# Kernel tuning notes

Measured on AMD Instinct MI355X. Metric: run time of the kernel, lower is better.

Reference implementation:

```python
import jax, jax.numpy as jnp
import numpy as np

NUM_ITERATIONS = 3


def squash(s, axis):
    # s: capsule vectors; squash along `axis` (capsule dim)
    mag_sq = jnp.sum(s * s, axis=axis, keepdims=True)
    mag = jnp.sqrt(mag_sq)
    return mag_sq / (1.0 + mag_sq) * (s / mag)


def setup_inputs() -> dict:
    key = jax.random.key(0)
    k1, k2 = jax.random.split(key)
    B, IN_SIZE, I = 256, 8, 1152   # batch, in_size, in_node_num
    N, O = 10, 16                  # num_node, node_size
    x = jax.random.normal(k1, (B, IN_SIZE, I), dtype=jnp.float32)
    W = jax.random.normal(k2, (1, I, N, O, IN_SIZE), dtype=jnp.float32)
    return {"x": x, "W": W}


def reference(x, W):
    # x: (B, in_size, I); W: (1, I, N, O, in_size)
    B = x.shape[0]
    I, N = W.shape[1], W.shape[2]
    xt = jnp.swapaxes(x, 1, 2)  # (B, I, in_size)
    # u_hat[b,i,n,o] = sum_k (0.03*W[0,i,n,o,k]) * x[b,i,k]
    u_hat = jnp.einsum('inok,bik->bino', W[0] * 0.03, xt)  # (B, I, N, O)
    b_ij = jnp.zeros((I, N), dtype=x.dtype)
    v_j = None
    for _ in range(NUM_ITERATIONS):
        c_ij = jax.nn.softmax(b_ij, axis=1)              # softmax over num_node
        s_j = jnp.einsum('in,bino->bno', c_ij, u_hat)    # (B, N, O)
        v_j = squash(s_j, axis=-1)                       # squash over node_size
        # agreement: u_hat . v_j, averaged over batch
        u_vj = jnp.einsum('bino,bno->bin', u_hat, v_j).mean(axis=0)  # (I, N)
        b_ij = b_ij + u_vj
    return v_j[:, :, :, None]  # (B, N, O, 1) == v_j.squeeze(1) in torch
```

## Files before the change

### kernel.cpp

```cpp
#include <hip/hip_runtime.h>

#define B_   256
#define I_   1152
#define N_   10
#define P_   9216
#define NO_  160

typedef unsigned short u16;
typedef short s8v __attribute__((ext_vector_type(8)));
typedef float f4v __attribute__((ext_vector_type(4)));

__device__ inline float bf2f(u16 u){
  unsigned v = ((unsigned)u) << 16; float f; __builtin_memcpy(&f, &v, 4); return f;
}
__device__ inline u16 f2bf(float f){
  unsigned b; __builtin_memcpy(&b, &f, 4);
  b += 0x7fffu + ((b >> 16) & 1u);
  return (u16)(b >> 16);
}

__global__ void k_prep(const float* __restrict__ x, const float* __restrict__ W,
                       u16* __restrict__ xbp, u16* __restrict__ xpb,
                       u16* __restrict__ Wt, float* __restrict__ bij){
  __shared__ float tile[32][36];
  int t = threadIdx.x, u = blockIdx.x;
  if (u < 160){
    if (u < 45) bij[u*256 + t] = 0.f;
    int q = u, n = q >> 4, o = q & 15;
    for (int i0 = 0; i0 < I_; i0 += 256){
      int i = i0 + t;
      if (i < I_){
        const float* src = W + (size_t)i*1280 + n*128 + o*8;
        float4 a = *reinterpret_cast<const float4*>(src);
        float4 b = *reinterpret_cast<const float4*>(src + 4);
        float vv[8] = {a.x,a.y,a.z,a.w,b.x,b.y,b.z,b.w};
        #pragma unroll
        for (int k = 0; k < 8; ++k)
          Wt[(size_t)q*P_ + (size_t)k*I_ + i] = f2bf(vv[k] * 0.03f);
      }
    }
  } else {
    int b2 = u - 160;
    int tb = b2 & 7, tp = b2 >> 3;
    int b0 = tb << 5, p0 = tp << 5;
    int r = t >> 3, c4 = (t & 7) << 2;
    float4 v = *reinterpret_cast<const float4*>(x + (size_t)(b0 + r)*P_ + p0 + c4);
    *reinterpret_cast<float4*>(&tile[r][c4]) = v;
    uint2 pk;
    pk.x = (unsigned)f2bf(v.x) | ((unsigned)f2bf(v.y) << 16);
    pk.y = (unsigned)f2bf(v.z) | ((unsigned)f2bf(v.w) << 16);
    *reinterpret_cast<uint2*>(xbp + (size_t)(b0 + r)*P_ + p0 + c4) = pk;
    __syncthreads();
    float f0 = tile[c4+0][r], f1 = tile[c4+1][r], f2 = tile[c4+2][r], f3 = tile[c4+3][r];
    uint2 pk2;
    pk2.x = (unsigned)f2bf(f0) | ((unsigned)f2bf(f1) << 16);
    pk2.y = (unsigned)f2bf(f2) | ((unsigned)f2bf(f3) << 16);
    *reinterpret_cast<uint2*>(xpb + (size_t)(p0 + r)*B_ + b0 + c4) = pk2;
  }
}

__global__ __launch_bounds__(128) void k_s2(
    const u16* __restrict__ xbp, const u16* __restrict__ Wt,
    const float* __restrict__ bij, float* __restrict__ s_part){
  __shared__ u16  Bt[16][584];
  __shared__ float c_lds[576];
  int t = threadIdx.x;
  int bx2 = blockIdx.x, n = blockIdx.y, kc = blockIdx.z;
  int i0 = (kc & 1) * 576;

  for (int j = t; j < 576; j += 128){
    const float* br = bij + (size_t)(i0 + j)*N_;
    float l0 = br[0], l1 = br[1], l2 = br[2], l3 = br[3], l4 = br[4];
    float l5 = br[5], l6 = br[6], l7 = br[7], l8 = br[8], l9 = br[9];
    float mx = fmaxf(fmaxf(fmaxf(fmaxf(l0,l1),fmaxf(l2,l3)),
                           fmaxf(fmaxf(l4,l5),fmaxf(l6,l7))), fmaxf(l8,l9));
    float e0=__expf(l0-mx), e1=__expf(l1-mx), e2=__expf(l2-mx), e3=__expf(l3-mx), e4=__expf(l4-mx);
    float e5=__expf(l5-mx), e6=__expf(l6-mx), e7=__expf(l7-mx), e8=__expf(l8-mx), e9=__expf(l9-mx);
    float se = e0+e1+e2+e3+e4+e5+e6+e7+e8+e9;
    float ev[10] = {e0,e1,e2,e3,e4,e5,e6,e7,e8,e9};
    c_lds[j] = ev[n] / se;
  }
  __syncthreads();

  for (int u = t; u < 1152; u += 128){
    int r = u / 72, cb = (u - r*72) * 8;
    uint4 w = *reinterpret_cast<const uint4*>(Wt + (size_t)(n*16 + r)*P_ + kc*576 + cb);
    float4 c0 = *reinterpret_cast<const float4*>(&c_lds[cb]);
    float4 c1 = *reinterpret_cast<const float4*>(&c_lds[cb + 4]);
    uint4 rr;
    rr.x = (unsigned)f2bf(bf2f(w.x & 0xffff)*c0.x) | ((unsigned)f2bf(bf2f(w.x >> 16)*c0.y) << 16);
    rr.y = (unsigned)f2bf(bf2f(w.y & 0xffff)*c0.z) | ((unsigned)f2bf(bf2f(w.y >> 16)*c0.w) << 16);
    rr.z = (unsigned)f2bf(bf2f(w.z & 0xffff)*c1.x) | ((unsigned)f2bf(bf2f(w.z >> 16)*c1.y) << 16);
    rr.w = (unsigned)f2bf(bf2f(w.w & 0xffff)*c1.z) | ((unsigned)f2bf(bf2f(w.w >> 16)*c1.w) << 16);
    *reinterpret_cast<uint4*>(&Bt[r][cb]) = rr;
  }
  __syncthreads();

  int w = t >> 6, l = t & 63;
  int lo = l & 15, quad = l >> 4;
  int b0 = bx2*32 + w*16;
  const s8v* ap = reinterpret_cast<const s8v*>(xbp + (size_t)(b0 + lo)*P_ + kc*576 + quad*8);
  f4v acc0 = {0.f,0.f,0.f,0.f}, acc1 = {0.f,0.f,0.f,0.f};
  #pragma unroll
  for (int s = 0; s < 9; ++s){
    s8v a0 = ap[8*s];
    s8v b0v = *reinterpret_cast<const s8v*>(&Bt[lo][quad*8 + 64*s]);
    s8v a1 = ap[8*s + 4];
    s8v b1v = *reinterpret_cast<const s8v*>(&Bt[lo][quad*8 + 64*s + 32]);
    acc0 = __builtin_amdgcn_mfma_f32_16x16x32_bf16(a0, b0v, acc0, 0, 0, 0);
    acc1 = __builtin_amdgcn_mfma_f32_16x16x32_bf16(a1, b1v, acc1, 0, 0, 0);
  }
  f4v acc = acc0 + acc1;
  float* op = s_part + (size_t)kc*40960;
  int r0 = quad << 2;
  #pragma unroll
  for (int r = 0; r < 4; ++r)
    op[(size_t)(b0 + r0 + r)*NO_ + n*16 + lo] = acc[r];
}

__global__ void k_sq(const float* __restrict__ s_part, float* __restrict__ out,
                     u16* __restrict__ vbt){
  int t = threadIdx.x;
  int o = t & 15, rl = t >> 4;
  int rowid = blockIdx.x*16 + rl;
  int b = rowid / 10, n = rowid - b*10;
  size_t idx = (size_t)b*NO_ + n*16 + o;
  float sv = 0.f;
  #pragma unroll
  for (int c = 0; c < 16; ++c) sv += s_part[idx + (size_t)c*40960];
  float sq = sv * sv;
  #pragma unroll
  for (int m = 8; m >= 1; m >>= 1) sq += __shfl_xor(sq, m, 16);
  float outv = sv * sqrtf(sq) / (1.0f + sq);
  out[idx] = outv;
  vbt[(size_t)(n*16 + o)*B_ + b] = f2bf(outv);
}

__global__ void k_g(const u16* __restrict__ xpb, const u16* __restrict__ vbt,
                    const u16* __restrict__ Wt, float* __restrict__ bij){
  int w = blockIdx.x*4 + (threadIdx.x >> 6);
  int l = threadIdx.x & 63;
  int pt = w % 576, qp = w / 576;
  int p0 = pt << 4;
  int lo = l & 15, quad = l >> 4;
  const s8v* ap  = reinterpret_cast<const s8v*>(xpb + (size_t)(p0 + lo)*B_ + quad*8);
  const s8v* bp0 = reinterpret_cast<const s8v*>(vbt + (size_t)((qp*2+0)*16 + lo)*B_ + quad*8);
  const s8v* bp1 = reinterpret_cast<const s8v*>(vbt + (size_t)((qp*2+1)*16 + lo)*B_ + quad*8);
  f4v acc0 = {0.f,0.f,0.f,0.f}, acc1 = {0.f,0.f,0.f,0.f};
  #pragma unroll
  for (int s = 0; s < 8; ++s){
    s8v a  = ap[4*s];
    s8v b0 = bp0[4*s];
    s8v b1 = bp1[4*s];
    acc0 = __builtin_amdgcn_mfma_f32_16x16x32_bf16(a, b0, acc0, 0, 0, 0);
    acc1 = __builtin_amdgcn_mfma_f32_16x16x32_bf16(a, b1, acc1, 0, 0, 0);
  }
  int ib = p0 % 1152;
  #pragma unroll
  for (int s = 0; s < 2; ++s){
    f4v acc = s ? acc1 : acc0;
    int n = qp*2 + s;
    const u16* wp = Wt + (size_t)(n*16 + lo)*P_ + p0 + (quad << 2);
    ushort4 w4 = *reinterpret_cast<const ushort4*>(wp);
    float v0 = acc[0]*bf2f(w4.x), v1 = acc[1]*bf2f(w4.y);
    float v2 = acc[2]*bf2f(w4.z), v3 = acc[3]*bf2f(w4.w);
    #pragma unroll
    for (int m = 8; m >= 1; m >>= 1){
      v0 += __shfl_xor(v0, m, 16);
      v1 += __shfl_xor(v1, m, 16);
      v2 += __shfl_xor(v2, m, 16);
      v3 += __shfl_xor(v3, m, 16);
    }
    if (lo == 0){
      int i = ib + (quad << 2);
      atomicAdd(&bij[(i+0)*N_ + n], v0 * (1.f/256.f));
      atomicAdd(&bij[(i+1)*N_ + n], v1 * (1.f/256.f));
      atomicAdd(&bij[(i+2)*N_ + n], v2 * (1.f/256.f));
      atomicAdd(&bij[(i+3)*N_ + n], v3 * (1.f/256.f));
    }
  }
}

extern "C" void kernel_launch(void* const* d_in, const int* in_sizes, int n_in,
                              void* d_out, int out_size, void* d_ws, size_t ws_size,
                              hipStream_t stream){
  (void)in_sizes; (void)n_in; (void)out_size; (void)ws_size;
  const float* x = (const float*)d_in[0];
  const float* W = (const float*)d_in[1];
  float* out = (float*)d_out;

  float* s_part = (float*)d_ws;
  float* bij    = s_part + 16*40960;
  u16* xbp = (u16*)(bij + 11520);
  u16* xpb = xbp + 2359296;
  u16* Wt  = xpb + 2359296;
  u16* vbt = Wt  + 1474560;

  k_prep<<<2464, 256, 0, stream>>>(x, W, xbp, xpb, Wt, bij);
  for (int it = 0; it < 3; ++it){
    k_s2<<<dim3(8, 10, 16), 128, 0, stream>>>(xbp, Wt, bij, s_part);
    k_sq<<<160, 256, 0, stream>>>(s_part, out, vbt);
    if (it < 2)
      k_g<<<720, 256, 0, stream>>>(xpb, vbt, Wt, bij);
  }
}
```

Measured before the change: 143.2 us.

## Process two capsule nodes per s2 block and split W prep across more blocks

k_s2 now computes two output nodes per block, so each A fragment loaded from global xbp is reused for two sets of MFMAs. This halves the number of blocks and the redundant softmax and x traffic. k_prep splits each W row's transpose over five blocks instead of one looping block, which should give more parallelism in the prep phase. In exchange, LDS per block roughly doubles and the grid shrinks to 640 blocks, which may reduce occupancy and latency hiding.

```diff
diff --git a/kernel.cpp b/kernel.cpp
--- a/kernel.cpp
+++ b/kernel.cpp
@@ -24,23 +24,22 @@
                        u16* __restrict__ Wt, float* __restrict__ bij){
   __shared__ float tile[32][36];
   int t = threadIdx.x, u = blockIdx.x;
-  if (u < 160){
+  if (u < 800){
     if (u < 45) bij[u*256 + t] = 0.f;
-    int q = u, n = q >> 4, o = q & 15;
-    for (int i0 = 0; i0 < I_; i0 += 256){
-      int i = i0 + t;
-      if (i < I_){
-        const float* src = W + (size_t)i*1280 + n*128 + o*8;
-        float4 a = *reinterpret_cast<const float4*>(src);
-        float4 b = *reinterpret_cast<const float4*>(src + 4);
-        float vv[8] = {a.x,a.y,a.z,a.w,b.x,b.y,b.z,b.w};
-        #pragma unroll
-        for (int k = 0; k < 8; ++k)
-          Wt[(size_t)q*P_ + (size_t)k*I_ + i] = f2bf(vv[k] * 0.03f);
-      }
+    int q = u / 5, ic = u - (u/5)*5;
+    int n = q >> 4, o = q & 15;
+    int i = ic*256 + t;
+    if (i < I_){
+      const float* src = W + (size_t)i*1280 + n*128 + o*8;
+      float4 a = *reinterpret_cast<const float4*>(src);
+      float4 b = *reinterpret_cast<const float4*>(src + 4);
+      float vv[8] = {a.x,a.y,a.z,a.w,b.x,b.y,b.z,b.w};
+      #pragma unroll
+      for (int k = 0; k < 8; ++k)
+        Wt[(size_t)q*P_ + (size_t)k*I_ + i] = f2bf(vv[k] * 0.03f);
     }
   } else {
-    int b2 = u - 160;
+    int b2 = u - 800;
     int tb = b2 & 7, tp = b2 >> 3;
     int b0 = tb << 5, p0 = tp << 5;
     int r = t >> 3, c4 = (t & 7) << 2;
@@ -62,10 +61,10 @@
 __global__ __launch_bounds__(128) void k_s2(
     const u16* __restrict__ xbp, const u16* __restrict__ Wt,
     const float* __restrict__ bij, float* __restrict__ s_part){
-  __shared__ u16  Bt[16][584];
-  __shared__ float c_lds[576];
+  __shared__ u16  Bt[2][16][592];
+  __shared__ float c2[2][576];
   int t = threadIdx.x;
-  int bx2 = blockIdx.x, n = blockIdx.y, kc = blockIdx.z;
+  int bx2 = blockIdx.x, np = blockIdx.y, kc = blockIdx.z;
   int i0 = (kc & 1) * 576;
 
   for (int j = t; j < 576; j += 128){
@@ -77,22 +76,26 @@
     float e0=__expf(l0-mx), e1=__expf(l1-mx), e2=__expf(l2-mx), e3=__expf(l3-mx), e4=__expf(l4-mx);
     float e5=__expf(l5-mx), e6=__expf(l6-mx), e7=__expf(l7-mx), e8=__expf(l8-mx), e9=__expf(l9-mx);
     float se = e0+e1+e2+e3+e4+e5+e6+e7+e8+e9;
+    float inv = 1.f / se;
     float ev[10] = {e0,e1,e2,e3,e4,e5,e6,e7,e8,e9};
-    c_lds[j] = ev[n] / se;
+    c2[0][j] = ev[np*2]   * inv;
+    c2[1][j] = ev[np*2+1] * inv;
   }
   __syncthreads();
 
-  for (int u = t; u < 1152; u += 128){
-    int r = u / 72, cb = (u - r*72) * 8;
-    uint4 w = *reinterpret_cast<const uint4*>(Wt + (size_t)(n*16 + r)*P_ + kc*576 + cb);
-    float4 c0 = *reinterpret_cast<const float4*>(&c_lds[cb]);
-    float4 c1 = *reinterpret_cast<const float4*>(&c_lds[cb + 4]);
+  for (int u = t; u < 2304; u += 128){
+    int nn = u / 1152, rem = u - nn*1152;
+    int r = rem / 72, cb = (rem - r*72) * 8;
+    int q = (np*2 + nn)*16 + r;
+    uint4 w = *reinterpret_cast<const uint4*>(Wt + (size_t)q*P_ + kc*576 + cb);
+    float4 c0 = *reinterpret_cast<const float4*>(&c2[nn][cb]);
+    float4 c1 = *reinterpret_cast<const float4*>(&c2[nn][cb + 4]);
     uint4 rr;
     rr.x = (unsigned)f2bf(bf2f(w.x & 0xffff)*c0.x) | ((unsigned)f2bf(bf2f(w.x >> 16)*c0.y) << 16);
     rr.y = (unsigned)f2bf(bf2f(w.y & 0xffff)*c0.z) | ((unsigned)f2bf(bf2f(w.y >> 16)*c0.w) << 16);
     rr.z = (unsigned)f2bf(bf2f(w.z & 0xffff)*c1.x) | ((unsigned)f2bf(bf2f(w.z >> 16)*c1.y) << 16);
     rr.w = (unsigned)f2bf(bf2f(w.w & 0xffff)*c1.z) | ((unsigned)f2bf(bf2f(w.w >> 16)*c1.w) << 16);
-    *reinterpret_cast<uint4*>(&Bt[r][cb]) = rr;
+    *reinterpret_cast<uint4*>(&Bt[nn][r][cb]) = rr;
   }
   __syncthreads();
 
@@ -100,22 +103,30 @@
   int lo = l & 15, quad = l >> 4;
   int b0 = bx2*32 + w*16;
   const s8v* ap = reinterpret_cast<const s8v*>(xbp + (size_t)(b0 + lo)*P_ + kc*576 + quad*8);
-  f4v acc0 = {0.f,0.f,0.f,0.f}, acc1 = {0.f,0.f,0.f,0.f};
+  f4v a00 = {0.f,0.f,0.f,0.f}, a01 = {0.f,0.f,0.f,0.f};
+  f4v a10 = {0.f,0.f,0.f,0.f}, a11 = {0.f,0.f,0.f,0.f};
   #pragma unroll
   for (int s = 0; s < 9; ++s){
-    s8v a0 = ap[8*s];
-    s8v b0v = *reinterpret_cast<const s8v*>(&Bt[lo][quad*8 + 64*s]);
-    s8v a1 = ap[8*s + 4];
-    s8v b1v = *reinterpret_cast<const s8v*>(&Bt[lo][quad*8 + 64*s + 32]);
-    acc0 = __builtin_amdgcn_mfma_f32_16x16x32_bf16(a0, b0v, acc0, 0, 0, 0);
-    acc1 = __builtin_amdgcn_mfma_f32_16x16x32_bf16(a1, b1v, acc1, 0, 0, 0);
-  }
-  f4v acc = acc0 + acc1;
+    s8v av0 = ap[8*s];
+    s8v av1 = ap[8*s + 4];
+    s8v b00 = *reinterpret_cast<const s8v*>(&Bt[0][lo][quad*8 + 64*s]);
+    s8v b01 = *reinterpret_cast<const s8v*>(&Bt[0][lo][quad*8 + 64*s + 32]);
+    s8v b10 = *reinterpret_cast<const s8v*>(&Bt[1][lo][quad*8 + 64*s]);
+    s8v b11 = *reinterpret_cast<const s8v*>(&Bt[1][lo][quad*8 + 64*s + 32]);
+    a00 = __builtin_amdgcn_mfma_f32_16x16x32_bf16(av0, b00, a00, 0, 0, 0);
+    a01 = __builtin_amdgcn_mfma_f32_16x16x32_bf16(av1, b01, a01, 0, 0, 0);
+    a10 = __builtin_amdgcn_mfma_f32_16x16x32_bf16(av0, b10, a10, 0, 0, 0);
+    a11 = __builtin_amdgcn_mfma_f32_16x16x32_bf16(av1, b11, a11, 0, 0, 0);
+  }
+  f4v accA = a00 + a01;
+  f4v accB = a10 + a11;
   float* op = s_part + (size_t)kc*40960;
   int r0 = quad << 2;
   #pragma unroll
-  for (int r = 0; r < 4; ++r)
-    op[(size_t)(b0 + r0 + r)*NO_ + n*16 + lo] = acc[r];
+  for (int r = 0; r < 4; ++r){
+    op[(size_t)(b0 + r0 + r)*NO_ + (np*2+0)*16 + lo] = accA[r];
+    op[(size_t)(b0 + r0 + r)*NO_ + (np*2+1)*16 + lo] = accB[r];
+  }
 }
 
 __global__ void k_sq(const float* __restrict__ s_part, float* __restrict__ out,
@@ -196,9 +207,9 @@
   u16* Wt  = xpb + 2359296;
   u16* vbt = Wt  + 1474560;
 
-  k_prep<<<2464, 256, 0, stream>>>(x, W, xbp, xpb, Wt, bij);
+  k_prep<<<3104, 256, 0, stream>>>(x, W, xbp, xpb, Wt, bij);
   for (int it = 0; it < 3; ++it){
-    k_s2<<<dim3(8, 10, 16), 128, 0, stream>>>(xbp, Wt, bij, s_part);
+    k_s2<<<dim3(8, 5, 16), 128, 0, stream>>>(xbp, Wt, bij, s_part);
     k_sq<<<160, 256, 0, stream>>>(s_part, out, vbt);
     if (it < 2)
       k_g<<<720, 256, 0, stream>>>(xpb, vbt, Wt, bij);
```

Result: slower. 148.6 us (+3.8%).

## Fuse squash into agreement kernel and reduce s partials with atomics

Applied to the files above, without the earlier changes.

The s_j partial sums are now accumulated with atomicAdd into a single double-buffered s array instead of 16 partial slices. Each s2 launch zeroes the next buffer, and the standalone squash kernel is removed from the loop. The agreement kernel computes the squash itself and stages v in LDS as bf16. The W prep is spread over more blocks. This cuts kernel launches and the extra partial-sum traffic, at the cost of atomic contention and redundant squash work repeated in every k_g2 block.

```diff
diff --git a/kernel.cpp b/kernel.cpp
--- a/kernel.cpp
+++ b/kernel.cpp
@@ -21,26 +21,27 @@
 
 __global__ void k_prep(const float* __restrict__ x, const float* __restrict__ W,
                        u16* __restrict__ xbp, u16* __restrict__ xpb,
-                       u16* __restrict__ Wt, float* __restrict__ bij){
+                       u16* __restrict__ Wt, float* __restrict__ bij,
+                       float* __restrict__ sA){
   __shared__ float tile[32][36];
   int t = threadIdx.x, u = blockIdx.x;
-  if (u < 160){
+  if (u < 800){
     if (u < 45) bij[u*256 + t] = 0.f;
-    int q = u, n = q >> 4, o = q & 15;
-    for (int i0 = 0; i0 < I_; i0 += 256){
-      int i = i0 + t;
-      if (i < I_){
-        const float* src = W + (size_t)i*1280 + n*128 + o*8;
-        float4 a = *reinterpret_cast<const float4*>(src);
-        float4 b = *reinterpret_cast<const float4*>(src + 4);
-        float vv[8] = {a.x,a.y,a.z,a.w,b.x,b.y,b.z,b.w};
-        #pragma unroll
-        for (int k = 0; k < 8; ++k)
-          Wt[(size_t)q*P_ + (size_t)k*I_ + i] = f2bf(vv[k] * 0.03f);
-      }
+    else if (u < 205) sA[(u - 45)*256 + t] = 0.f;
+    int q = u / 5, ic = u - (u/5)*5;
+    int n = q >> 4, o = q & 15;
+    int i = ic*256 + t;
+    if (i < I_){
+      const float* src = W + (size_t)i*1280 + n*128 + o*8;
+      float4 a = *reinterpret_cast<const float4*>(src);
+      float4 b = *reinterpret_cast<const float4*>(src + 4);
+      float vv[8] = {a.x,a.y,a.z,a.w,b.x,b.y,b.z,b.w};
+      #pragma unroll
+      for (int k = 0; k < 8; ++k)
+        Wt[(size_t)q*P_ + (size_t)k*I_ + i] = f2bf(vv[k] * 0.03f);
     }
   } else {
-    int b2 = u - 160;
+    int b2 = u - 800;
     int tb = b2 & 7, tp = b2 >> 3;
     int b0 = tb << 5, p0 = tp << 5;
     int r = t >> 3, c4 = (t & 7) << 2;
@@ -59,13 +60,16 @@
   }
 }
 
-__global__ __launch_bounds__(128) void k_s2(
+__global__ __launch_bounds__(128) void k_s2a(
     const u16* __restrict__ xbp, const u16* __restrict__ Wt,
-    const float* __restrict__ bij, float* __restrict__ s_part){
-  __shared__ u16  Bt[16][584];
+    const float* __restrict__ bij, float* __restrict__ s_cur,
+    float* __restrict__ s_next){
+  __shared__ u16  Bt[16][592];
   __shared__ float c_lds[576];
   int t = threadIdx.x;
   int bx2 = blockIdx.x, n = blockIdx.y, kc = blockIdx.z;
+  int lin = bx2 + 8*n + 80*kc;
+  if (t < 32) s_next[lin*32 + t] = 0.f;
   int i0 = (kc & 1) * 576;
 
   for (int j = t; j < 576; j += 128){
@@ -111,55 +115,58 @@
     acc1 = __builtin_amdgcn_mfma_f32_16x16x32_bf16(a1, b1v, acc1, 0, 0, 0);
   }
   f4v acc = acc0 + acc1;
-  float* op = s_part + (size_t)kc*40960;
   int r0 = quad << 2;
   #pragma unroll
   for (int r = 0; r < 4; ++r)
-    op[(size_t)(b0 + r0 + r)*NO_ + n*16 + lo] = acc[r];
-}
-
-__global__ void k_sq(const float* __restrict__ s_part, float* __restrict__ out,
-                     u16* __restrict__ vbt){
+    atomicAdd(&s_cur[(size_t)(b0 + r0 + r)*NO_ + n*16 + lo], acc[r]);
+}
+
+__global__ __launch_bounds__(256, 4) void k_g2(
+    const u16* __restrict__ xpb, const float* __restrict__ s,
+    const u16* __restrict__ Wt, float* __restrict__ bij){
+  __shared__ u16 vl[32][264];
   int t = threadIdx.x;
-  int o = t & 15, rl = t >> 4;
-  int rowid = blockIdx.x*16 + rl;
-  int b = rowid / 10, n = rowid - b*10;
-  size_t idx = (size_t)b*NO_ + n*16 + o;
-  float sv = 0.f;
-  #pragma unroll
-  for (int c = 0; c < 16; ++c) sv += s_part[idx + (size_t)c*40960];
-  float sq = sv * sv;
-  #pragma unroll
-  for (int m = 8; m >= 1; m >>= 1) sq += __shfl_xor(sq, m, 16);
-  float outv = sv * sqrtf(sq) / (1.0f + sq);
-  out[idx] = outv;
-  vbt[(size_t)(n*16 + o)*B_ + b] = f2bf(outv);
-}
-
-__global__ void k_g(const u16* __restrict__ xpb, const u16* __restrict__ vbt,
-                    const u16* __restrict__ Wt, float* __restrict__ bij){
-  int w = blockIdx.x*4 + (threadIdx.x >> 6);
-  int l = threadIdx.x & 63;
-  int pt = w % 576, qp = w / 576;
+  int qp = blockIdx.x / 144;
+  int b = t;
+  #pragma unroll
+  for (int nn = 0; nn < 2; ++nn){
+    const float* sr = s + (size_t)b*NO_ + (qp*2 + nn)*16;
+    float4 s0 = *reinterpret_cast<const float4*>(sr);
+    float4 s1 = *reinterpret_cast<const float4*>(sr + 4);
+    float4 s2 = *reinterpret_cast<const float4*>(sr + 8);
+    float4 s3 = *reinterpret_cast<const float4*>(sr + 12);
+    float sq = s0.x*s0.x+s0.y*s0.y+s0.z*s0.z+s0.w*s0.w
+             + s1.x*s1.x+s1.y*s1.y+s1.z*s1.z+s1.w*s1.w
+             + s2.x*s2.x+s2.y*s2.y+s2.z*s2.z+s2.w*s2.w
+             + s3.x*s3.x+s3.y*s3.y+s3.z*s3.z+s3.w*s3.w;
+    float scale = sqrtf(sq) / (1.0f + sq);
+    float sv[16] = {s0.x,s0.y,s0.z,s0.w,s1.x,s1.y,s1.z,s1.w,
+                    s2.x,s2.y,s2.z,s2.w,s3.x,s3.y,s3.z,s3.w};
+    #pragma unroll
+    for (int o = 0; o < 16; ++o)
+      vl[nn*16 + o][b] = f2bf(sv[o] * scale);
+  }
+  __syncthreads();
+
+  int wv = t >> 6, l = t & 63;
+  int pt = (blockIdx.x % 144)*4 + wv;
   int p0 = pt << 4;
   int lo = l & 15, quad = l >> 4;
-  const s8v* ap  = reinterpret_cast<const s8v*>(xpb + (size_t)(p0 + lo)*B_ + quad*8);
-  const s8v* bp0 = reinterpret_cast<const s8v*>(vbt + (size_t)((qp*2+0)*16 + lo)*B_ + quad*8);
-  const s8v* bp1 = reinterpret_cast<const s8v*>(vbt + (size_t)((qp*2+1)*16 + lo)*B_ + quad*8);
+  const s8v* ap = reinterpret_cast<const s8v*>(xpb + (size_t)(p0 + lo)*B_ + quad*8);
   f4v acc0 = {0.f,0.f,0.f,0.f}, acc1 = {0.f,0.f,0.f,0.f};
   #pragma unroll
-  for (int s = 0; s < 8; ++s){
-    s8v a  = ap[4*s];
-    s8v b0 = bp0[4*s];
-    s8v b1 = bp1[4*s];
+  for (int st = 0; st < 8; ++st){
+    s8v a  = ap[4*st];
+    s8v b0 = *reinterpret_cast<const s8v*>(&vl[lo]     [st*32 + quad*8]);
+    s8v b1 = *reinterpret_cast<const s8v*>(&vl[16 + lo][st*32 + quad*8]);
     acc0 = __builtin_amdgcn_mfma_f32_16x16x32_bf16(a, b0, acc0, 0, 0, 0);
     acc1 = __builtin_amdgcn_mfma_f32_16x16x32_bf16(a, b1, acc1, 0, 0, 0);
   }
   int ib = p0 % 1152;
   #pragma unroll
-  for (int s = 0; s < 2; ++s){
-    f4v acc = s ? acc1 : acc0;
-    int n = qp*2 + s;
+  for (int sb = 0; sb < 2; ++sb){
+    f4v acc = sb ? acc1 : acc0;
+    int n = qp*2 + sb;
     const u16* wp = Wt + (size_t)(n*16 + lo)*P_ + p0 + (quad << 2);
     ushort4 w4 = *reinterpret_cast<const ushort4*>(wp);
     float v0 = acc[0]*bf2f(w4.x), v1 = acc[1]*bf2f(w4.y);
@@ -181,6 +188,19 @@
   }
 }
 
+__global__ void k_sqout(const float* __restrict__ s, float* __restrict__ out){
+  int t = threadIdx.x;
+  int o = t & 15, rl = t >> 4;
+  int rowid = blockIdx.x*16 + rl;
+  int b = rowid / 10, n = rowid - b*10;
+  size_t idx = (size_t)b*NO_ + n*16 + o;
+  float sv = s[idx];
+  float sq = sv * sv;
+  #pragma unroll
+  for (int m = 8; m >= 1; m >>= 1) sq += __shfl_xor(sq, m, 16);
+  out[idx] = sv * sqrtf(sq) / (1.0f + sq);
+}
+
 extern "C" void kernel_launch(void* const* d_in, const int* in_sizes, int n_in,
                               void* d_out, int out_size, void* d_ws, size_t ws_size,
                               hipStream_t stream){
@@ -189,18 +209,18 @@
   const float* W = (const float*)d_in[1];
   float* out = (float*)d_out;
 
-  float* s_part = (float*)d_ws;
-  float* bij    = s_part + 16*40960;
+  float* sA  = (float*)d_ws;
+  float* sB  = sA + 40960;
+  float* bij = sB + 40960;
   u16* xbp = (u16*)(bij + 11520);
   u16* xpb = xbp + 2359296;
   u16* Wt  = xpb + 2359296;
-  u16* vbt = Wt  + 1474560;
-
-  k_prep<<<2464, 256, 0, stream>>>(x, W, xbp, xpb, Wt, bij);
-  for (int it = 0; it < 3; ++it){
-    k_s2<<<dim3(8, 10, 16), 128, 0, stream>>>(xbp, Wt, bij, s_part);
-    k_sq<<<160, 256, 0, stream>>>(s_part, out, vbt);
-    if (it < 2)
-      k_g<<<720, 256, 0, stream>>>(xpb, vbt, Wt, bij);
-  }
-}
+
+  k_prep<<<3104, 256, 0, stream>>>(x, W, xbp, xpb, Wt, bij, sA);
+  k_s2a<<<dim3(8, 10, 16), 128, 0, stream>>>(xbp, Wt, bij, sA, sB);
+  k_g2 <<<720, 256, 0, stream>>>(xpb, sA, Wt, bij);
+  k_s2a<<<dim3(8, 10, 16), 128, 0, stream>>>(xbp, Wt, bij, sB, sA);
+  k_g2 <<<720, 256, 0, stream>>>(xpb, sB, Wt, bij);
+  k_s2a<<<dim3(8, 10, 16), 128, 0, stream>>>(xbp, Wt, bij, sA, sB);
+  k_sqout<<<160, 256, 0, stream>>>(sA, out);
+}
```

After: 132.8 us, median of 2. 7.3% less time.
